# Kernel optimization log

Hardware: AMD Instinct MI355X
Metric: run time of the kernel (lower is better)

The kernel has to match this reference:

```python
import jax, jax.numpy as jnp
import numpy as np

IN_FEATURES = 4096
OUT_FEATURES = 4096
ALPHA = 0.002
BETA = 0.01


def setup_inputs() -> dict:
    key = jax.random.key(0)
    k_x, k_w, k_b = jax.random.split(key, 3)
    # int8 activations, weights, bias (matching torch.randint(-127, 127, ...))
    x = jax.random.randint(k_x, (4, 2048, IN_FEATURES), -127, 127, dtype=jnp.int32).astype(jnp.int8)
    weight = jax.random.randint(k_w, (OUT_FEATURES, IN_FEATURES), -127, 127, dtype=jnp.int32).astype(jnp.int8)
    bias = jax.random.randint(k_b, (1, OUT_FEATURES), -127, 127, dtype=jnp.int32).astype(jnp.int8)
    a = jnp.float32(ALPHA)
    b = jnp.float32(BETA)
    return {"x": x, "weight": weight, "bias": bias, "a": a, "b": b}


def reference(x, weight, bias, a, b):
    # int8 bias add, and requantize-to-int8 epilogue.
    x_shape = x.shape
    x2d = x.reshape(-1, x_shape[-1])                       # [M, K] int8
    # int32 accumulation: acc = x @ W^T
    acc = jnp.matmul(x2d.astype(jnp.int32), weight.T.astype(jnp.int32),
                     preferred_element_type=jnp.int32)      # [M, N] int32
    # epilogue: alpha * acc + beta * bias, round + clamp to int8 range
    y = a * acc.astype(jnp.float32) + b * bias.astype(jnp.float32)
    y = jnp.clip(jnp.round(y), -128.0, 127.0).astype(jnp.int8)
    return y.reshape(*x_shape[:-1], -1)
```

## Files before the change

### kernel.cpp

```cpp
#include <hip/hip_runtime.h>

#define K_DIM 4096
#define N_DIM 4096

typedef int v4i __attribute__((ext_vector_type(4)));

__device__ __forceinline__ void gload_lds16(const void* g, void* l) {
  __builtin_amdgcn_global_load_lds(
      (const __attribute__((address_space(1))) void*)g,
      (__attribute__((address_space(3))) void*)l, 16, 0, 0);
}

__device__ __forceinline__ int pack4(int4 w) {
  return (w.x & 0xff) | ((w.y & 0xff) << 8) | ((w.z & 0xff) << 16) | (w.w << 24);
}

__global__ __launch_bounds__(256) void pack_kernel(const int* __restrict__ src,
                                                   int4* __restrict__ dst, int n16) {
  int i = blockIdx.x * 256 + threadIdx.x;
  if (i >= n16) return;
  const int4* s = (const int4*)src + (size_t)i * 4;
  int4 w0 = s[0], w1 = s[1], w2 = s[2], w3 = s[3];
  int4 r;
  r.x = pack4(w0); r.y = pack4(w1); r.z = pack4(w2); r.w = pack4(w3);
  dst[i] = r;
}

template <bool PACKED>
__global__ __launch_bounds__(256, 2) void gemm_i8(
    const void* __restrict__ Asrc, const void* __restrict__ Bsrc,
    const int* __restrict__ bias, const float* __restrict__ pa,
    const float* __restrict__ pb, int* __restrict__ out, int gridM) {
  __shared__ __align__(16) char As[128 * 128];
  __shared__ __align__(16) char Bs[128 * 128];

  const int tid = threadIdx.x;
  const int wid = tid >> 6;
  const int lane = tid & 63;

  const int nwg = gridM * 32;
  const int cpx = nwg >> 3;
  const int flat = blockIdx.x;
  const int wg = (flat & 7) * cpx + (flat >> 3);
  const int br = wg >> 5;
  const int bn = wg & 31;

  const int rowi = tid >> 3;
  const int swzc = (tid & 7) ^ (rowi & 7);

  v4i acc[4][4];
  {
    v4i z = {0, 0, 0, 0};
#pragma unroll
    for (int mi = 0; mi < 4; ++mi)
#pragma unroll
      for (int ni = 0; ni < 4; ++ni) acc[mi][ni] = z;
  }

  const int wr = wid >> 1;
  const int wc = wid & 1;

  const char* Ag = (const char*)Asrc + (size_t)(br * 128 + rowi) * K_DIM + swzc * 16;
  const char* Bg = (const char*)Bsrc + (size_t)(bn * 128 + rowi) * K_DIM + swzc * 16;

  for (int ks = 0; ks < K_DIM / 128; ++ks) {
    if constexpr (PACKED) {
      const char* a0 = Ag + ks * 128;
      const char* b0 = Bg + ks * 128;
#pragma unroll
      for (int is = 0; is < 4; ++is) {
        gload_lds16(a0 + (size_t)is * 32 * K_DIM, &As[is * 4096 + wid * 1024]);
        gload_lds16(b0 + (size_t)is * 32 * K_DIM, &Bs[is * 4096 + wid * 1024]);
      }
    } else {
      const int* Ai = (const int*)Asrc;
      const int* Bi = (const int*)Bsrc;
#pragma unroll
      for (int is = 0; is < 4; ++is) {
        {
          const int4* p = (const int4*)(Ai + (size_t)(br * 128 + is * 32 + rowi) * K_DIM +
                                        ks * 128 + swzc * 16);
          int4 w0 = p[0], w1 = p[1], w2 = p[2], w3 = p[3];
          v4i r = {pack4(w0), pack4(w1), pack4(w2), pack4(w3)};
          *(v4i*)&As[is * 4096 + tid * 16] = r;
        }
        {
          const int4* p = (const int4*)(Bi + (size_t)(bn * 128 + is * 32 + rowi) * K_DIM +
                                        ks * 128 + swzc * 16);
          int4 w0 = p[0], w1 = p[1], w2 = p[2], w3 = p[3];
          v4i r = {pack4(w0), pack4(w1), pack4(w2), pack4(w3)};
          *(v4i*)&Bs[is * 4096 + tid * 16] = r;
        }
      }
    }
    __syncthreads();

#pragma unroll
    for (int ksub = 0; ksub < 2; ++ksub) {
      const int g = lane >> 4;
      const int kk = ksub * 4 + g;
      v4i af[4], bf[4];
#pragma unroll
      for (int mi = 0; mi < 4; ++mi) {
        const int r = wr * 64 + mi * 16 + (lane & 15);
        af[mi] = *(const v4i*)&As[r * 128 + ((kk ^ (r & 7)) * 16)];
      }
#pragma unroll
      for (int ni = 0; ni < 4; ++ni) {
        const int r = wc * 64 + ni * 16 + (lane & 15);
        bf[ni] = *(const v4i*)&Bs[r * 128 + ((kk ^ (r & 7)) * 16)];
      }
#pragma unroll
      for (int mi = 0; mi < 4; ++mi)
#pragma unroll
        for (int ni = 0; ni < 4; ++ni)
          acc[mi][ni] =
              __builtin_amdgcn_mfma_i32_16x16x64_i8(af[mi], bf[ni], acc[mi][ni], 0, 0, 0);
    }
    __syncthreads();
  }

  const float alpha = *pa;
  const float beta = *pb;
  const int col = lane & 15;
  const int rg = lane >> 4;
#pragma unroll
  for (int ni = 0; ni < 4; ++ni) {
    const int n = bn * 128 + wc * 64 + ni * 16 + col;
    const float bb = __fmul_rn(beta, (float)bias[n]);
#pragma unroll
    for (int mi = 0; mi < 4; ++mi) {
#pragma unroll
      for (int j = 0; j < 4; ++j) {
        const int m = br * 128 + wr * 64 + mi * 16 + rg * 4 + j;
        float y = __fadd_rn(__fmul_rn(alpha, (float)acc[mi][ni][j]), bb);
        y = rintf(y);
        y = fminf(127.f, fmaxf(-128.f, y));
        out[(size_t)m * N_DIM + n] = (int)y;
      }
    }
  }
}

extern "C" void kernel_launch(void* const* d_in, const int* in_sizes, int n_in,
                              void* d_out, int out_size, void* d_ws, size_t ws_size,
                              hipStream_t stream) {
  const int* x = (const int*)d_in[0];
  const int* w = (const int*)d_in[1];
  const int* bias = (const int*)d_in[2];
  const float* pa = (const float*)d_in[3];
  const float* pb = (const float*)d_in[4];
  int* out = (int*)d_out;

  const int M = in_sizes[0] / K_DIM;
  const int gridM = M / 128;
  const size_t xBytes = (size_t)M * K_DIM;
  const size_t wBytes = (size_t)N_DIM * K_DIM;

  if (ws_size >= xBytes + wBytes) {
    char* xp = (char*)d_ws;
    char* wp = xp + xBytes;
    const int n16x = (int)(xBytes / 16);
    const int n16w = (int)(wBytes / 16);
    pack_kernel<<<(n16x + 255) / 256, 256, 0, stream>>>(x, (int4*)xp, n16x);
    pack_kernel<<<(n16w + 255) / 256, 256, 0, stream>>>(w, (int4*)wp, n16w);
    gemm_i8<true><<<gridM * 32, 256, 0, stream>>>(xp, wp, bias, pa, pb, out, gridM);
  } else {
    gemm_i8<false><<<gridM * 32, 256, 0, stream>>>(x, w, bias, pa, pb, out, gridM);
  }
}
```

Baseline: 210.3 us.

## Use 256x256 tiles with 4-stage async LDS pipeline and 8 waves

Replaces the 128x128, 256-thread GEMM with a 256x256 tile computed by 512 threads (8 waves) and a 4-deep ring of 64-wide K slices in 128KB of dynamic LDS. Global-to-LDS loads are issued three stages ahead with explicit vmcnt waits and split barriers, and MFMA bursts run at raised wave priority so the load issue interleaves with compute. The intent is to raise arithmetic intensity per loaded byte and hide memory latency, at the cost of lower occupancy (128KB LDS per block) and removal of the fallback path when the workspace is too small.

```diff
diff --git a/kernel.cpp b/kernel.cpp
--- a/kernel.cpp
+++ b/kernel.cpp
@@ -2,6 +2,7 @@
 
 #define K_DIM 4096
 #define N_DIM 4096
+#define NT (K_DIM / 64)
 
 typedef int v4i __attribute__((ext_vector_type(4)));
 
@@ -26,98 +27,105 @@
   dst[i] = r;
 }
 
-template <bool PACKED>
-__global__ __launch_bounds__(256, 2) void gemm_i8(
-    const void* __restrict__ Asrc, const void* __restrict__ Bsrc,
+__global__ __launch_bounds__(512, 2) void gemm256(
+    const char* __restrict__ Ap, const char* __restrict__ Bp,
     const int* __restrict__ bias, const float* __restrict__ pa,
-    const float* __restrict__ pb, int* __restrict__ out, int gridM) {
-  __shared__ __align__(16) char As[128 * 128];
-  __shared__ __align__(16) char Bs[128 * 128];
+    const float* __restrict__ pb, int* __restrict__ out) {
+  extern __shared__ __align__(16) char lds[];
 
   const int tid = threadIdx.x;
   const int wid = tid >> 6;
   const int lane = tid & 63;
 
-  const int nwg = gridM * 32;
+  const int nwg = gridDim.x;
   const int cpx = nwg >> 3;
   const int flat = blockIdx.x;
   const int wg = (flat & 7) * cpx + (flat >> 3);
-  const int br = wg >> 5;
-  const int bn = wg & 31;
+  const int br = wg >> 4;
+  const int bn = wg & 15;
 
-  const int rowi = tid >> 3;
-  const int swzc = (tid & 7) ^ (rowi & 7);
+  const int wr = wid >> 2;
+  const int wcol = wid & 3;
 
-  v4i acc[4][4];
+  const int srow = tid >> 2;
+  const int schunk = (tid & 3) ^ ((tid >> 3) & 3);
+  const char* aSrc = Ap + (size_t)(br * 256 + srow) * K_DIM + schunk * 16;
+  const char* bSrc = Bp + (size_t)(bn * 256 + srow) * K_DIM + schunk * 16;
+  char* const ldsA = lds;
+  char* const ldsB = lds + 65536;
+
+  auto stageA = [&](int kt) {
+    const char* s = aSrc + kt * 64;
+    char* d = ldsA + (kt & 3) * 16384 + wid * 1024;
+    gload_lds16(s, d);
+    gload_lds16(s + (size_t)128 * K_DIM, d + 8192);
+  };
+  auto stageB = [&](int kt) {
+    const char* s = bSrc + kt * 64;
+    char* d = ldsB + (kt & 3) * 16384 + wid * 1024;
+    gload_lds16(s, d);
+    gload_lds16(s + (size_t)128 * K_DIM, d + 8192);
+  };
+
+  const int lrow = lane & 15;
+  const int fchunk = lane >> 4;
+  const int rchunk = fchunk ^ ((lrow >> 1) & 3);
+  const int aOff = (wr * 128 + lrow) * 64 + rchunk * 16;
+  const int bOff = 65536 + (wcol * 64 + lrow) * 64 + rchunk * 16;
+
+  v4i acc[8][4];
   {
     v4i z = {0, 0, 0, 0};
 #pragma unroll
-    for (int mi = 0; mi < 4; ++mi)
+    for (int mi = 0; mi < 8; ++mi)
 #pragma unroll
       for (int ni = 0; ni < 4; ++ni) acc[mi][ni] = z;
   }
 
-  const int wr = wid >> 1;
-  const int wc = wid & 1;
+  stageA(0); stageB(0);
+  stageA(1); stageB(1);
+  stageA(2); stageB(2);
 
-  const char* Ag = (const char*)Asrc + (size_t)(br * 128 + rowi) * K_DIM + swzc * 16;
-  const char* Bg = (const char*)Bsrc + (size_t)(bn * 128 + rowi) * K_DIM + swzc * 16;
+  for (int kt = 0; kt < NT; ++kt) {
+    if (kt < NT - 2)
+      asm volatile("s_waitcnt vmcnt(8)" ::: "memory");
+    else if (kt == NT - 2)
+      asm volatile("s_waitcnt vmcnt(4)" ::: "memory");
+    else
+      asm volatile("s_waitcnt vmcnt(0)" ::: "memory");
+    __builtin_amdgcn_s_barrier();
 
-  for (int ks = 0; ks < K_DIM / 128; ++ks) {
-    if constexpr (PACKED) {
-      const char* a0 = Ag + ks * 128;
-      const char* b0 = Bg + ks * 128;
+    const int sb = (kt & 3) * 16384;
+
+    v4i af[4], bf[4];
 #pragma unroll
-      for (int is = 0; is < 4; ++is) {
-        gload_lds16(a0 + (size_t)is * 32 * K_DIM, &As[is * 4096 + wid * 1024]);
-        gload_lds16(b0 + (size_t)is * 32 * K_DIM, &Bs[is * 4096 + wid * 1024]);
-      }
-    } else {
-      const int* Ai = (const int*)Asrc;
-      const int* Bi = (const int*)Bsrc;
+    for (int mi = 0; mi < 4; ++mi) af[mi] = *(const v4i*)&lds[sb + aOff + mi * 1024];
 #pragma unroll
-      for (int is = 0; is < 4; ++is) {
-        {
-          const int4* p = (const int4*)(Ai + (size_t)(br * 128 + is * 32 + rowi) * K_DIM +
-                                        ks * 128 + swzc * 16);
-          int4 w0 = p[0], w1 = p[1], w2 = p[2], w3 = p[3];
-          v4i r = {pack4(w0), pack4(w1), pack4(w2), pack4(w3)};
-          *(v4i*)&As[is * 4096 + tid * 16] = r;
-        }
-        {
-          const int4* p = (const int4*)(Bi + (size_t)(bn * 128 + is * 32 + rowi) * K_DIM +
-                                        ks * 128 + swzc * 16);
-          int4 w0 = p[0], w1 = p[1], w2 = p[2], w3 = p[3];
-          v4i r = {pack4(w0), pack4(w1), pack4(w2), pack4(w3)};
-          *(v4i*)&Bs[is * 4096 + tid * 16] = r;
-        }
-      }
-    }
-    __syncthreads();
+    for (int ni = 0; ni < 4; ++ni) bf[ni] = *(const v4i*)&lds[sb + bOff + ni * 1024];
+    if (kt < NT - 3) stageA(kt + 3);
+    __builtin_amdgcn_s_barrier();
+    __builtin_amdgcn_s_setprio(1);
+#pragma unroll
+    for (int mi = 0; mi < 4; ++mi)
+#pragma unroll
+      for (int ni = 0; ni < 4; ++ni)
+        acc[mi][ni] =
+            __builtin_amdgcn_mfma_i32_16x16x64_i8(af[mi], bf[ni], acc[mi][ni], 0, 0, 0);
+    __builtin_amdgcn_s_setprio(0);
 
+    v4i af2[4];
 #pragma unroll
-    for (int ksub = 0; ksub < 2; ++ksub) {
-      const int g = lane >> 4;
-      const int kk = ksub * 4 + g;
-      v4i af[4], bf[4];
+    for (int mi = 0; mi < 4; ++mi) af2[mi] = *(const v4i*)&lds[sb + aOff + (mi + 4) * 1024];
+    if (kt < NT - 3) stageB(kt + 3);
+    __builtin_amdgcn_s_barrier();
+    __builtin_amdgcn_s_setprio(1);
 #pragma unroll
-      for (int mi = 0; mi < 4; ++mi) {
-        const int r = wr * 64 + mi * 16 + (lane & 15);
-        af[mi] = *(const v4i*)&As[r * 128 + ((kk ^ (r & 7)) * 16)];
-      }
+    for (int mi = 0; mi < 4; ++mi)
 #pragma unroll
-      for (int ni = 0; ni < 4; ++ni) {
-        const int r = wc * 64 + ni * 16 + (lane & 15);
-        bf[ni] = *(const v4i*)&Bs[r * 128 + ((kk ^ (r & 7)) * 16)];
-      }
-#pragma unroll
-      for (int mi = 0; mi < 4; ++mi)
-#pragma unroll
-        for (int ni = 0; ni < 4; ++ni)
-          acc[mi][ni] =
-              __builtin_amdgcn_mfma_i32_16x16x64_i8(af[mi], bf[ni], acc[mi][ni], 0, 0, 0);
-    }
-    __syncthreads();
+      for (int ni = 0; ni < 4; ++ni)
+        acc[mi + 4][ni] =
+            __builtin_amdgcn_mfma_i32_16x16x64_i8(af2[mi], bf[ni], acc[mi + 4][ni], 0, 0, 0);
+    __builtin_amdgcn_s_setprio(0);
   }
 
   const float alpha = *pa;
@@ -126,13 +134,13 @@
   const int rg = lane >> 4;
 #pragma unroll
   for (int ni = 0; ni < 4; ++ni) {
-    const int n = bn * 128 + wc * 64 + ni * 16 + col;
+    const int n = bn * 256 + wcol * 64 + ni * 16 + col;
     const float bb = __fmul_rn(beta, (float)bias[n]);
 #pragma unroll
-    for (int mi = 0; mi < 4; ++mi) {
+    for (int mi = 0; mi < 8; ++mi) {
 #pragma unroll
       for (int j = 0; j < 4; ++j) {
-        const int m = br * 128 + wr * 64 + mi * 16 + rg * 4 + j;
+        const int m = br * 256 + wr * 128 + mi * 16 + rg * 4 + j;
         float y = __fadd_rn(__fmul_rn(alpha, (float)acc[mi][ni][j]), bb);
         y = rintf(y);
         y = fminf(127.f, fmaxf(-128.f, y));
@@ -153,19 +161,18 @@
   int* out = (int*)d_out;
 
   const int M = in_sizes[0] / K_DIM;
-  const int gridM = M / 128;
   const size_t xBytes = (size_t)M * K_DIM;
   const size_t wBytes = (size_t)N_DIM * K_DIM;
 
-  if (ws_size >= xBytes + wBytes) {
-    char* xp = (char*)d_ws;
-    char* wp = xp + xBytes;
-    const int n16x = (int)(xBytes / 16);
-    const int n16w = (int)(wBytes / 16);
-    pack_kernel<<<(n16x + 255) / 256, 256, 0, stream>>>(x, (int4*)xp, n16x);
-    pack_kernel<<<(n16w + 255) / 256, 256, 0, stream>>>(w, (int4*)wp, n16w);
-    gemm_i8<true><<<gridM * 32, 256, 0, stream>>>(xp, wp, bias, pa, pb, out, gridM);
-  } else {
-    gemm_i8<false><<<gridM * 32, 256, 0, stream>>>(x, w, bias, pa, pb, out, gridM);
-  }
+  char* xp = (char*)d_ws;
+  char* wp = xp + xBytes;
+  const int n16x = (int)(xBytes / 16);
+  const int n16w = (int)(wBytes / 16);
+  pack_kernel<<<(n16x + 255) / 256, 256, 0, stream>>>(x, (int4*)xp, n16x);
+  pack_kernel<<<(n16w + 255) / 256, 256, 0, stream>>>(w, (int4*)wp, n16w);
+
+  const int nwg = (M / 256) * (N_DIM / 256);
+  hipFuncSetAttribute((const void*)gemm256,
+                      hipFuncAttributeMaxDynamicSharedMemorySize, 131072);
+  gemm256<<<nwg, 512, 131072, stream>>>(xp, wp, bias, pa, pb, out);
 }
```

Measured after the change: 196.9 us. 6.4% less time.
